# Performance work log

Measured on AMD Instinct MI355X. Metric: run time of the kernel, lower is better.

Reference implementation:

```python
import jax, jax.numpy as jnp
import numpy as np

N_NODES = 50000
N_EDGES = 800000
NFEAT, NHID, NOUT = 512, 256, 64


def setup_inputs() -> dict:
    key = jax.random.key(0)
    ks = jax.random.split(key, 8)
    x = jax.random.normal(ks[0], (N_NODES, NFEAT), dtype=jnp.float32)
    w1 = jax.random.normal(ks[1], (NFEAT, NHID), dtype=jnp.float32) * (1.0 / np.sqrt(NFEAT))
    b1 = jnp.zeros((NHID,), dtype=jnp.float32)
    w2 = jax.random.normal(ks[2], (NHID, NOUT), dtype=jnp.float32) * (1.0 / np.sqrt(NHID))
    b2 = jnp.zeros((NOUT,), dtype=jnp.float32)
    edge_w = jax.random.uniform(ks[3], (N_EDGES,), dtype=jnp.float32)
    row = jnp.sort(jax.random.randint(ks[4], (N_EDGES,), 0, N_NODES, dtype=jnp.int32))
    col = jax.random.randint(ks[5], (N_EDGES,), 0, N_NODES, dtype=jnp.int32)
    return {"x": x, "w1": w1, "b1": b1, "w2": w2, "b2": b2,
            "edge_w": edge_w, "row": row, "col": col}


def _spmm(edge_w, row, col, h, n_nodes):
    # sparse adj (COO) @ dense h : gather source rows, scale, scatter-add to dest
    msgs = h[col] * edge_w[:, None]          # [E, d]
    return jax.ops.segment_sum(msgs, row, num_segments=n_nodes)


def reference(x, w1, b1, w2, b2, edge_w, row, col):
    n = x.shape[0]
    # layer 1: support = x @ W1; out = adj @ support + b1; relu
    h = jnp.matmul(x, w1)                    # [N, nhid]
    h = _spmm(edge_w, row, col, h, n) + b1
    h = jax.nn.relu(h)
    # layer 2
    h = jnp.matmul(h, w2)                    # [N, nout]
    out = _spmm(edge_w, row, col, h, n) + b2
    return out
```

## Files before the change

### kernel.cpp

```cpp
#include <hip/hip_runtime.h>

#define N_NODES 50000
#define MP      50048
#define N_EDGES 800000
#define NFEAT   512
#define NHID    256
#define NOUT    64

typedef __bf16 bf16x8 __attribute__((ext_vector_type(8)));
typedef float  f32x4  __attribute__((ext_vector_type(4)));

#define GLOAD_LDS16(g, l) __builtin_amdgcn_global_load_lds(                    \
    (const __attribute__((address_space(1))) void*)(g),                        \
    (__attribute__((address_space(3))) void*)(l), 16, 0, 0)

__device__ __forceinline__ unsigned short f2bf(float f) {
    __bf16 b = (__bf16)f;
    return __builtin_bit_cast(unsigned short, b);
}

__global__ __launch_bounds__(256) void prep(const int* __restrict__ row,
                                            int* __restrict__ rp,
                                            const float* __restrict__ w1,
                                            __bf16* __restrict__ w1t,
                                            const float* __restrict__ w2,
                                            __bf16* __restrict__ w2t,
                                            __bf16* __restrict__ h1) {
    const int b = blockIdx.x, t = threadIdx.x;
    if (b < 196) {
        int r = b * 256 + t;
        if (r <= N_NODES) {
            int lo = 0, hi = N_EDGES;
            while (lo < hi) {
                int mid = (lo + hi) >> 1;
                if (row[mid] < r) lo = mid + 1; else hi = mid;
            }
            rp[r] = lo;
        }
    } else if (b < 708) {
        int o = (b - 196) * 256 + t;
        w1t[o] = (__bf16)w1[(size_t)(o & 511) * NHID + (o >> 9)];
    } else if (b < 772) {
        int o = (b - 708) * 256 + t;
        w2t[o] = (__bf16)w2[(size_t)(o & 255) * NOUT + (o >> 8)];
    } else {
        int o = (b - 772) * 256 + t;
        h1[(size_t)N_NODES * NHID + o] = (__bf16)0.f;
    }
}

__global__ __launch_bounds__(256) void gemm1_fused(const float* __restrict__ X,
                                                   const __bf16* __restrict__ Bt,
                                                   __bf16* __restrict__ C) {
    __shared__ __bf16 As[64 * 32];
    __shared__ __bf16 Bs[256 * 32];
    const int t = threadIdx.x;
    const int w = t >> 6, l = t & 63;
    const int wm = w >> 1, wn = w & 1;
    const int ml = l & 15, quad = l >> 4;
    const int row0 = blockIdx.x * 64;

    const int ar = t >> 2;
    const int ac = (t & 3) * 8;
    const int agr = row0 + ar;
    const bool aval = (agr < N_NODES);
    const float* asrc = X + (size_t)agr * NFEAT + ac;

    f32x4 acc[2][8] = {};

    float4 pa = make_float4(0.f, 0.f, 0.f, 0.f), pb = pa;
    if (aval) { pa = *(const float4*)asrc; pb = *(const float4*)(asrc + 4); }

    for (int k0 = 0; k0 < NFEAT; k0 += 32) {
        #pragma unroll
        for (int it = 0; it < 4; it++) {
            int q = it * 256 + w * 64 + l;
            int r = q >> 2, cc = (q & 3) * 8;
            GLOAD_LDS16(Bt + (size_t)r * NFEAT + k0 + cc,
                        Bs + (size_t)(it * 256 + w * 64) * 8);
        }
        {
            uint4 o;
            o.x = (unsigned)f2bf(pa.x) | ((unsigned)f2bf(pa.y) << 16);
            o.y = (unsigned)f2bf(pa.z) | ((unsigned)f2bf(pa.w) << 16);
            o.z = (unsigned)f2bf(pb.x) | ((unsigned)f2bf(pb.y) << 16);
            o.w = (unsigned)f2bf(pb.z) | ((unsigned)f2bf(pb.w) << 16);
            *(uint4*)(As + (size_t)t * 8) = o;
        }
        __syncthreads();

        if (k0 + 32 < NFEAT && aval) {
            pa = *(const float4*)(asrc + k0 + 32);
            pb = *(const float4*)(asrc + k0 + 36);
        }

        bf16x8 af[2], bfr[8];
        #pragma unroll
        for (int mi = 0; mi < 2; mi++)
            af[mi] = *(const bf16x8*)(As + (wm * 32 + mi * 16 + ml) * 32 + quad * 8);
        #pragma unroll
        for (int ni = 0; ni < 8; ni++)
            bfr[ni] = *(const bf16x8*)(Bs + (wn * 128 + ni * 16 + ml) * 32 + quad * 8);
        #pragma unroll
        for (int mi = 0; mi < 2; mi++)
            #pragma unroll
            for (int ni = 0; ni < 8; ni++)
                acc[mi][ni] = __builtin_amdgcn_mfma_f32_16x16x32_bf16(
                    af[mi], bfr[ni], acc[mi][ni], 0, 0, 0);
        __syncthreads();
    }

    #pragma unroll
    for (int mi = 0; mi < 2; mi++) {
        int gr = row0 + wm * 32 + mi * 16 + quad * 4;
        #pragma unroll
        for (int ni = 0; ni < 8; ni++) {
            int gc = wn * 128 + ni * 16 + ml;
            #pragma unroll
            for (int r2 = 0; r2 < 4; r2++)
                C[(size_t)(gr + r2) * NHID + gc] = (__bf16)acc[mi][ni][r2];
        }
    }
}

__global__ __launch_bounds__(256) void gemm2_mfma(const __bf16* __restrict__ A,
                                                  const __bf16* __restrict__ Bt,
                                                  __bf16* __restrict__ C) {
    __shared__ __bf16 As[128 * 32];
    __shared__ __bf16 Bs[64 * 32];
    const int t = threadIdx.x;
    const int w = t >> 6, l = t & 63;
    const int ml = l & 15, quad = l >> 4;
    const int row0 = blockIdx.x * 128;

    f32x4 acc[2][4] = {};

    for (int k0 = 0; k0 < NHID; k0 += 32) {
        #pragma unroll
        for (int i = 0; i < 2; i++) {
            int q = (w * 2 + i) * 64 + l;
            int r = q >> 2, cc = (q & 3) * 8;
            GLOAD_LDS16(A + (size_t)(row0 + r) * NHID + k0 + cc, As + (w * 2 + i) * 512);
        }
        {
            int q = w * 64 + l;
            int r = q >> 2, cc = (q & 3) * 8;
            GLOAD_LDS16(Bt + (size_t)r * NHID + k0 + cc, Bs + w * 512);
        }
        __syncthreads();
        bf16x8 af[2], bfr[4];
        #pragma unroll
        for (int mi = 0; mi < 2; mi++)
            af[mi] = *(const bf16x8*)(As + (w * 32 + mi * 16 + ml) * 32 + quad * 8);
        #pragma unroll
        for (int ni = 0; ni < 4; ni++)
            bfr[ni] = *(const bf16x8*)(Bs + (ni * 16 + ml) * 32 + quad * 8);
        #pragma unroll
        for (int mi = 0; mi < 2; mi++)
            #pragma unroll
            for (int ni = 0; ni < 4; ni++)
                acc[mi][ni] = __builtin_amdgcn_mfma_f32_16x16x32_bf16(
                    af[mi], bfr[ni], acc[mi][ni], 0, 0, 0);
        __syncthreads();
    }

    #pragma unroll
    for (int mi = 0; mi < 2; mi++) {
        int gr = row0 + w * 32 + mi * 16 + quad * 4;
        #pragma unroll
        for (int ni = 0; ni < 4; ni++) {
            int gc = ni * 16 + ml;
            #pragma unroll
            for (int r2 = 0; r2 < 4; r2++)
                C[(size_t)(gr + r2) * NOUT + gc] = (__bf16)acc[mi][ni][r2];
        }
    }
}

__global__ __launch_bounds__(256) void spmm1_wave(const __bf16* __restrict__ h0,
                                                  const float* __restrict__ ew,
                                                  const int* __restrict__ col,
                                                  const int* __restrict__ rp,
                                                  const float* __restrict__ b1,
                                                  __bf16* __restrict__ h1) {
    const int n    = blockIdx.x * 4 + (threadIdx.x >> 6);
    const int lane = threadIdx.x & 63;
    const int half = lane >> 5;
    const int fl   = lane & 31;
    const int s = rp[n], e = rp[n + 1];

    float acc[8] = {};
    int i = s + half;
    for (; i + 6 < e; i += 8) {
        int   c0 = col[i],     c1 = col[i + 2], c2 = col[i + 4], c3 = col[i + 6];
        float w0 = ew[i],      w1 = ew[i + 2],  w2 = ew[i + 4],  w3 = ew[i + 6];
        uint4 v0 = *(const uint4*)(h0 + (size_t)c0 * NHID + fl * 8);
        uint4 v1 = *(const uint4*)(h0 + (size_t)c1 * NHID + fl * 8);
        uint4 v2 = *(const uint4*)(h0 + (size_t)c2 * NHID + fl * 8);
        uint4 v3 = *(const uint4*)(h0 + (size_t)c3 * NHID + fl * 8);
        const unsigned* p0 = &v0.x; const unsigned* p1 = &v1.x;
        const unsigned* p2 = &v2.x; const unsigned* p3 = &v3.x;
        #pragma unroll
        for (int j = 0; j < 4; j++) {
            acc[2*j+0] += w0 * __builtin_bit_cast(float, p0[j] << 16)
                        + w1 * __builtin_bit_cast(float, p1[j] << 16)
                        + w2 * __builtin_bit_cast(float, p2[j] << 16)
                        + w3 * __builtin_bit_cast(float, p3[j] << 16);
            acc[2*j+1] += w0 * __builtin_bit_cast(float, p0[j] & 0xffff0000u)
                        + w1 * __builtin_bit_cast(float, p1[j] & 0xffff0000u)
                        + w2 * __builtin_bit_cast(float, p2[j] & 0xffff0000u)
                        + w3 * __builtin_bit_cast(float, p3[j] & 0xffff0000u);
        }
    }
    for (; i < e; i += 2) {
        int   c0 = col[i];
        float w0 = ew[i];
        uint4 v0 = *(const uint4*)(h0 + (size_t)c0 * NHID + fl * 8);
        const unsigned* p0 = &v0.x;
        #pragma unroll
        for (int j = 0; j < 4; j++) {
            acc[2*j+0] += w0 * __builtin_bit_cast(float, p0[j] << 16);
            acc[2*j+1] += w0 * __builtin_bit_cast(float, p0[j] & 0xffff0000u);
        }
    }

    #pragma unroll
    for (int j = 0; j < 8; j++)
        acc[j] += __shfl_down(acc[j], 32, 64);

    if (half == 0) {
        unsigned short u[8];
        #pragma unroll
        for (int j = 0; j < 8; j++) {
            float v = acc[j] + b1[fl * 8 + j];
            u[j] = f2bf(v > 0.f ? v : 0.f);
        }
        uint4 o;
        o.x = (unsigned)u[0] | ((unsigned)u[1] << 16);
        o.y = (unsigned)u[2] | ((unsigned)u[3] << 16);
        o.z = (unsigned)u[4] | ((unsigned)u[5] << 16);
        o.w = (unsigned)u[6] | ((unsigned)u[7] << 16);
        *(uint4*)(h1 + (size_t)n * NHID + fl * 8) = o;
    }
}

__global__ __launch_bounds__(256) void spmm2_wave(const __bf16* __restrict__ h2,
                                                  const float* __restrict__ ew,
                                                  const int* __restrict__ col,
                                                  const int* __restrict__ rp,
                                                  const float* __restrict__ b2,
                                                  float* __restrict__ out) {
    const int n    = blockIdx.x * 4 + (threadIdx.x >> 6);
    const int lane = threadIdx.x & 63;
    const int g    = lane >> 4;
    const int fl   = lane & 15;
    const int s = rp[n], e = rp[n + 1];

    float a0 = 0.f, a1 = 0.f, a2 = 0.f, a3 = 0.f;
    int i = s + g;
    for (; i + 4 < e; i += 8) {
        int   c0 = col[i];     float w0 = ew[i];
        int   c1 = col[i + 4]; float w1 = ew[i + 4];
        uint2 v0 = *(const uint2*)(h2 + (size_t)c0 * NOUT + fl * 4);
        uint2 v1 = *(const uint2*)(h2 + (size_t)c1 * NOUT + fl * 4);
        a0 += w0 * __builtin_bit_cast(float, v0.x << 16)
            + w1 * __builtin_bit_cast(float, v1.x << 16);
        a1 += w0 * __builtin_bit_cast(float, v0.x & 0xffff0000u)
            + w1 * __builtin_bit_cast(float, v1.x & 0xffff0000u);
        a2 += w0 * __builtin_bit_cast(float, v0.y << 16)
            + w1 * __builtin_bit_cast(float, v1.y << 16);
        a3 += w0 * __builtin_bit_cast(float, v0.y & 0xffff0000u)
            + w1 * __builtin_bit_cast(float, v1.y & 0xffff0000u);
    }
    for (; i < e; i += 4) {
        int   c0 = col[i]; float w0 = ew[i];
        uint2 v0 = *(const uint2*)(h2 + (size_t)c0 * NOUT + fl * 4);
        a0 += w0 * __builtin_bit_cast(float, v0.x << 16);
        a1 += w0 * __builtin_bit_cast(float, v0.x & 0xffff0000u);
        a2 += w0 * __builtin_bit_cast(float, v0.y << 16);
        a3 += w0 * __builtin_bit_cast(float, v0.y & 0xffff0000u);
    }

    a0 += __shfl_down(a0, 32, 64); a1 += __shfl_down(a1, 32, 64);
    a2 += __shfl_down(a2, 32, 64); a3 += __shfl_down(a3, 32, 64);
    a0 += __shfl_down(a0, 16, 64); a1 += __shfl_down(a1, 16, 64);
    a2 += __shfl_down(a2, 16, 64); a3 += __shfl_down(a3, 16, 64);

    if (lane < 16) {
        float4 bb = *(const float4*)(b2 + fl * 4);
        float4 o = make_float4(a0 + bb.x, a1 + bb.y, a2 + bb.z, a3 + bb.w);
        *(float4*)(out + (size_t)n * NOUT + fl * 4) = o;
    }
}

extern "C" void kernel_launch(void* const* d_in, const int* in_sizes, int n_in,
                              void* d_out, int out_size, void* d_ws, size_t ws_size,
                              hipStream_t stream) {
    const float* x   = (const float*)d_in[0];
    const float* w1  = (const float*)d_in[1];
    const float* b1  = (const float*)d_in[2];
    const float* w2  = (const float*)d_in[3];
    const float* b2  = (const float*)d_in[4];
    const float* ew  = (const float*)d_in[5];
    const int*   row = (const int*)d_in[6];
    const int*   col = (const int*)d_in[7];
    float* out = (float*)d_out;

    char* ws = (char*)d_ws;
    size_t off = 0;
    int*    rp  = (int*)(ws + off);   off += 256 * 1024;
    __bf16* w1t = (__bf16*)(ws + off); off += (size_t)NHID * NFEAT * 2;
    __bf16* w2t = (__bf16*)(ws + off); off += (size_t)NOUT * NHID * 2;
    __bf16* h0  = (__bf16*)(ws + off); off += (size_t)MP * NHID * 2;
    __bf16* h1  = (__bf16*)(ws + off); off += (size_t)MP * NHID * 2;
    __bf16* h2  = (__bf16*)(ws + off);

    prep<<<820, 256, 0, stream>>>(row, rp, w1, w1t, w2, w2t, h1);

    gemm1_fused<<<MP / 64, 256, 0, stream>>>(x, w1t, h0);

    spmm1_wave<<<N_NODES / 4, 256, 0, stream>>>(h0, ew, col, rp, b1, h1);

    gemm2_mfma<<<MP / 128, 256, 0, stream>>>(h1, w2t, h2);

    spmm2_wave<<<N_NODES / 4, 256, 0, stream>>>(h2, ew, col, rp, b2, out);
}
```

Before: 281.4 us.

## Load GEMM operands directly from global into MFMA registers, dropping LDS staging

Both dense GEMMs stop staging A and B tiles through shared memory with barriers. Each lane now loads its MFMA fragments straight from global memory: fp32 X rows are converted to bf16 in registers, and the transposed weight rows are read directly. gemm2 also shrinks its tile to 64 rows per block with one 16-row slice per wave. The intent is to remove LDS traffic and __syncthreads stalls, at the cost of redundant global and L2 reads of the weights across waves and less coalesced access patterns.

New measurement: 439.0 us. 56.0% more time.

```diff
diff --git a/kernel.cpp b/kernel.cpp
--- a/kernel.cpp
+++ b/kernel.cpp
@@ -10,13 +10,18 @@
 typedef __bf16 bf16x8 __attribute__((ext_vector_type(8)));
 typedef float  f32x4  __attribute__((ext_vector_type(4)));
 
-#define GLOAD_LDS16(g, l) __builtin_amdgcn_global_load_lds(                    \
-    (const __attribute__((address_space(1))) void*)(g),                        \
-    (__attribute__((address_space(3))) void*)(l), 16, 0, 0)
-
 __device__ __forceinline__ unsigned short f2bf(float f) {
     __bf16 b = (__bf16)f;
     return __builtin_bit_cast(unsigned short, b);
+}
+
+__device__ __forceinline__ bf16x8 pack8(float4 a, float4 b) {
+    uint4 o;
+    o.x = (unsigned)f2bf(a.x) | ((unsigned)f2bf(a.y) << 16);
+    o.y = (unsigned)f2bf(a.z) | ((unsigned)f2bf(a.w) << 16);
+    o.z = (unsigned)f2bf(b.x) | ((unsigned)f2bf(b.y) << 16);
+    o.w = (unsigned)f2bf(b.z) | ((unsigned)f2bf(b.w) << 16);
+    return __builtin_bit_cast(bf16x8, o);
 }
 
 __global__ __launch_bounds__(256) void prep(const int* __restrict__ row,
@@ -49,65 +54,44 @@
     }
 }
 
-__global__ __launch_bounds__(256) void gemm1_fused(const float* __restrict__ X,
-                                                   const __bf16* __restrict__ Bt,
-                                                   __bf16* __restrict__ C) {
-    __shared__ __bf16 As[64 * 32];
-    __shared__ __bf16 Bs[256 * 32];
+__global__ __launch_bounds__(256) void gemm1_direct(const float* __restrict__ X,
+                                                    const __bf16* __restrict__ Bt,
+                                                    __bf16* __restrict__ C) {
     const int t = threadIdx.x;
     const int w = t >> 6, l = t & 63;
     const int wm = w >> 1, wn = w & 1;
     const int ml = l & 15, quad = l >> 4;
     const int row0 = blockIdx.x * 64;
 
-    const int ar = t >> 2;
-    const int ac = (t & 3) * 8;
-    const int agr = row0 + ar;
-    const bool aval = (agr < N_NODES);
-    const float* asrc = X + (size_t)agr * NFEAT + ac;
+    const int m0 = row0 + wm * 32 + ml;
+    const bool v0 = (m0 < N_NODES);
+    const bool v1 = (m0 + 16 < N_NODES);
+    const float*  a0p = X  + (size_t)m0 * NFEAT + quad * 8;
+    const float*  a1p = a0p + (size_t)16 * NFEAT;
+    const __bf16* bp  = Bt + (size_t)(wn * 128 + ml) * NFEAT + quad * 8;
 
     f32x4 acc[2][8] = {};
-
-    float4 pa = make_float4(0.f, 0.f, 0.f, 0.f), pb = pa;
-    if (aval) { pa = *(const float4*)asrc; pb = *(const float4*)(asrc + 4); }
-
+    const float4 z4 = make_float4(0.f, 0.f, 0.f, 0.f);
+
+    #pragma unroll 2
     for (int k0 = 0; k0 < NFEAT; k0 += 32) {
-        #pragma unroll
-        for (int it = 0; it < 4; it++) {
-            int q = it * 256 + w * 64 + l;
-            int r = q >> 2, cc = (q & 3) * 8;
-            GLOAD_LDS16(Bt + (size_t)r * NFEAT + k0 + cc,
-                        Bs + (size_t)(it * 256 + w * 64) * 8);
-        }
-        {
-            uint4 o;
-            o.x = (unsigned)f2bf(pa.x) | ((unsigned)f2bf(pa.y) << 16);
-            o.y = (unsigned)f2bf(pa.z) | ((unsigned)f2bf(pa.w) << 16);
-            o.z = (unsigned)f2bf(pb.x) | ((unsigned)f2bf(pb.y) << 16);
-            o.w = (unsigned)f2bf(pb.z) | ((unsigned)f2bf(pb.w) << 16);
-            *(uint4*)(As + (size_t)t * 8) = o;
-        }
-        __syncthreads();
-
-        if (k0 + 32 < NFEAT && aval) {
-            pa = *(const float4*)(asrc + k0 + 32);
-            pb = *(const float4*)(asrc + k0 + 36);
-        }
-
-        bf16x8 af[2], bfr[8];
-        #pragma unroll
-        for (int mi = 0; mi < 2; mi++)
-            af[mi] = *(const bf16x8*)(As + (wm * 32 + mi * 16 + ml) * 32 + quad * 8);
+        float4 xa0 = v0 ? *(const float4*)(a0p + k0)     : z4;
+        float4 xb0 = v0 ? *(const float4*)(a0p + k0 + 4) : z4;
+        float4 xa1 = v1 ? *(const float4*)(a1p + k0)     : z4;
+        float4 xb1 = v1 ? *(const float4*)(a1p + k0 + 4) : z4;
+        bf16x8 bfr[8];
         #pragma unroll
         for (int ni = 0; ni < 8; ni++)
-            bfr[ni] = *(const bf16x8*)(Bs + (wn * 128 + ni * 16 + ml) * 32 + quad * 8);
+            bfr[ni] = *(const bf16x8*)(bp + (size_t)ni * 16 * NFEAT + k0);
+        bf16x8 af[2];
+        af[0] = pack8(xa0, xb0);
+        af[1] = pack8(xa1, xb1);
         #pragma unroll
         for (int mi = 0; mi < 2; mi++)
             #pragma unroll
             for (int ni = 0; ni < 8; ni++)
                 acc[mi][ni] = __builtin_amdgcn_mfma_f32_16x16x32_bf16(
                     af[mi], bfr[ni], acc[mi][ni], 0, 0, 0);
-        __syncthreads();
     }
 
     #pragma unroll
@@ -123,56 +107,39 @@
     }
 }
 
-__global__ __launch_bounds__(256) void gemm2_mfma(const __bf16* __restrict__ A,
-                                                  const __bf16* __restrict__ Bt,
-                                                  __bf16* __restrict__ C) {
-    __shared__ __bf16 As[128 * 32];
-    __shared__ __bf16 Bs[64 * 32];
+__global__ __launch_bounds__(256) void gemm2_direct(const __bf16* __restrict__ A,
+                                                    const __bf16* __restrict__ Bt,
+                                                    __bf16* __restrict__ C) {
     const int t = threadIdx.x;
     const int w = t >> 6, l = t & 63;
     const int ml = l & 15, quad = l >> 4;
-    const int row0 = blockIdx.x * 128;
-
-    f32x4 acc[2][4] = {};
-
+    const int row0 = blockIdx.x * 64;
+
+    const __bf16* ap = A  + (size_t)(row0 + w * 16 + ml) * NHID + quad * 8;
+    const __bf16* bp = Bt + (size_t)ml * NHID + quad * 8;
+
+    f32x4 acc[4] = {};
+
+    #pragma unroll
     for (int k0 = 0; k0 < NHID; k0 += 32) {
-        #pragma unroll
-        for (int i = 0; i < 2; i++) {
-            int q = (w * 2 + i) * 64 + l;
-            int r = q >> 2, cc = (q & 3) * 8;
-            GLOAD_LDS16(A + (size_t)(row0 + r) * NHID + k0 + cc, As + (w * 2 + i) * 512);
-        }
-        {
-            int q = w * 64 + l;
-            int r = q >> 2, cc = (q & 3) * 8;
-            GLOAD_LDS16(Bt + (size_t)r * NHID + k0 + cc, Bs + w * 512);
-        }
-        __syncthreads();
-        bf16x8 af[2], bfr[4];
-        #pragma unroll
-        for (int mi = 0; mi < 2; mi++)
-            af[mi] = *(const bf16x8*)(As + (w * 32 + mi * 16 + ml) * 32 + quad * 8);
+        bf16x8 af = *(const bf16x8*)(ap + k0);
+        bf16x8 bfr[4];
         #pragma unroll
         for (int ni = 0; ni < 4; ni++)
-            bfr[ni] = *(const bf16x8*)(Bs + (ni * 16 + ml) * 32 + quad * 8);
-        #pragma unroll
-        for (int mi = 0; mi < 2; mi++)
-            #pragma unroll
-            for (int ni = 0; ni < 4; ni++)
-                acc[mi][ni] = __builtin_amdgcn_mfma_f32_16x16x32_bf16(
-                    af[mi], bfr[ni], acc[mi][ni], 0, 0, 0);
-        __syncthreads();
-    }
-
-    #pragma unroll
-    for (int mi = 0; mi < 2; mi++) {
-        int gr = row0 + w * 32 + mi * 16 + quad * 4;
-        #pragma unroll
-        for (int ni = 0; ni < 4; ni++) {
-            int gc = ni * 16 + ml;
-            #pragma unroll
-            for (int r2 = 0; r2 < 4; r2++)
-                C[(size_t)(gr + r2) * NOUT + gc] = (__bf16)acc[mi][ni][r2];
+            bfr[ni] = *(const bf16x8*)(bp + (size_t)ni * 16 * NHID + k0);
+        #pragma unroll
+        for (int ni = 0; ni < 4; ni++)
+            acc[ni] = __builtin_amdgcn_mfma_f32_16x16x32_bf16(
+                af, bfr[ni], acc[ni], 0, 0, 0);
+    }
+
+    #pragma unroll
+    for (int ni = 0; ni < 4; ni++) {
+        int gc = ni * 16 + ml;
+        #pragma unroll
+        for (int r2 = 0; r2 < 4; r2++) {
+            int gr = row0 + w * 16 + quad * 4 + r2;
+            C[(size_t)gr * NOUT + gc] = (__bf16)acc[ni][r2];
         }
     }
 }
@@ -317,11 +284,11 @@
 
     prep<<<820, 256, 0, stream>>>(row, rp, w1, w1t, w2, w2t, h1);
 
-    gemm1_fused<<<MP / 64, 256, 0, stream>>>(x, w1t, h0);
+    gemm1_direct<<<MP / 64, 256, 0, stream>>>(x, w1t, h0);
 
     spmm1_wave<<<N_NODES / 4, 256, 0, stream>>>(h0, ew, col, rp, b1, h1);
 
-    gemm2_mfma<<<MP / 128, 256, 0, stream>>>(h1, w2t, h2);
+    gemm2_direct<<<MP / 64, 256, 0, stream>>>(h1, w2t, h2);
 
     spmm2_wave<<<N_NODES / 4, 256, 0, stream>>>(h2, ew, col, rp, b2, out);
 }
```
